# Kernel tuning notes

Measured on AMD Instinct MI355X. Metric: run time of the kernel, lower is better.

## Reference

```python
import jax, jax.numpy as jnp
import numpy as np

B, F_IN, NCH, T = 1, 1, 1536, 128
NW = [476, 476, 292]          # wires per plane (face 0)
NC = [10000, 10000, 10000]    # crossings per plane pair (01, 12, 20)
NCROSS = sum(NC)
E = 120000                    # ~4 nearest-neighbor edges per crossing node
N_FEAT_WIRE = 4
OUT_CH = 4
NODE_DIM = 2 * (F_IN + N_FEAT_WIRE) + 3  # = 13, matches GAT input dim


def setup_inputs() -> dict:
    key = jax.random.key(0)
    ks = jax.random.split(key, 18)
    x = jax.random.normal(ks[0], (B, F_IN, NCH, T), jnp.float32)
    chan_p0 = jax.random.randint(ks[1], (NW[0],), 0, NCH, jnp.int32)
    chan_p1 = jax.random.randint(ks[2], (NW[1],), 0, NCH, jnp.int32)
    chan_p2 = jax.random.randint(ks[3], (NW[2],), 0, NCH, jnp.int32)
    gidx_01 = jax.random.randint(ks[4], (NC[0], 2), 0, min(NW[0], NW[1]), jnp.int32)
    gidx_12 = jax.random.randint(ks[5], (NC[1], 2), 0, min(NW[1], NW[2]), jnp.int32)
    gidx_20 = jax.random.randint(ks[6], (NC[2], 2), 0, min(NW[2], NW[0]), jnp.int32)
    ray_01 = jax.random.normal(ks[7], (NC[0], 2), jnp.float32)
    ray_12 = jax.random.normal(ks[8], (NC[1], 2), jnp.float32)
    ray_20 = jax.random.normal(ks[9], (NC[2], 2), jnp.float32)
    edges = jax.random.randint(ks[10], (2, E), 0, NCROSS, jnp.int32)
    W_gat = jax.random.normal(ks[11], (NODE_DIM, OUT_CH), jnp.float32) * 0.1
    a_src = jax.random.normal(ks[12], (OUT_CH,), jnp.float32) * 0.1
    a_dst = jax.random.normal(ks[13], (OUT_CH,), jnp.float32) * 0.1
    b_gat = jnp.zeros((OUT_CH,), jnp.float32)
    W_mlp = jax.random.normal(ks[14], (OUT_CH, 1), jnp.float32) * 0.1
    b_mlp = jnp.zeros((1,), jnp.float32)
    return dict(x=x, chan_p0=chan_p0, chan_p1=chan_p1, chan_p2=chan_p2,
                gidx_01=gidx_01, gidx_12=gidx_12, gidx_20=gidx_20,
                ray_01=ray_01, ray_12=ray_12, ray_20=ray_20, edges=edges,
                W_gat=W_gat, a_src=a_src, a_dst=a_dst, b_gat=b_gat,
                W_mlp=W_mlp, b_mlp=b_mlp)


def _plane_feats(x, chan, plane_id):
    # x: [B,F,C,T] -> per-wire features [B,T,Nw,F+4]:
    # (signal, wire_ident, channel, 0, plane_id) -- mirrors as_wires_f0_pX.
    sig = jnp.transpose(x[:, :, chan, :], (0, 3, 2, 1))  # [B,T,Nw,F]
    nw = chan.shape[0]
    wire_id = jnp.arange(nw, dtype=jnp.float32)
    extra = jnp.stack([wire_id, chan.astype(jnp.float32),
                       jnp.zeros(nw, jnp.float32),
                       jnp.full((nw,), plane_id, jnp.float32)], axis=-1)  # [Nw,4]
    extra = jnp.broadcast_to(extra[None, None], sig.shape[:2] + extra.shape)
    return jnp.concatenate([sig, extra], axis=-1)


def _cross(fA, fB, gidx, rc):
    # crossing node features: wireA feats ++ wireB feats ++ ray xy ++ tick
    n = gidx.shape[0]
    tick = jnp.broadcast_to(jnp.arange(T, dtype=jnp.float32)[None, :, None, None],
                            (B, T, n, 1))
    rcb = jnp.broadcast_to(rc[None, None], (B, T, n, 2))
    return jnp.concatenate([fA[:, :, gidx[:, 0]], fB[:, :, gidx[:, 1]], rcb, tick],
                           axis=-1)  # [B,T,n,13]


def _gat_one(h, a_src, a_dst, src, dst):
    # single-graph, single-head GAT attention + aggregation. h: [N,OUT_CH]
    s = h @ a_src  # [N]
    d = h @ a_dst
    e = jax.nn.leaky_relu(s[src] + d[dst], 0.2)  # [E]
    m = jax.ops.segment_max(e, dst, num_segments=NCROSS)
    m = jnp.where(jnp.isfinite(m), m, 0.0)
    w = jnp.exp(e - m[dst])
    denom = jax.ops.segment_sum(w, dst, num_segments=NCROSS)
    msg = jax.ops.segment_sum(w[:, None] * h[src], dst, num_segments=NCROSS)
    return msg / (denom[:, None] + 1e-9)


def reference(x, chan_p0, chan_p1, chan_p2, gidx_01, gidx_12, gidx_20,
              ray_01, ray_12, ray_20, edges,
              W_gat, a_src, a_dst, b_gat, W_mlp, b_mlp):
    f0 = _plane_feats(x, chan_p0, 0.0)
    f1 = _plane_feats(x, chan_p1, 1.0)
    f2 = _plane_feats(x, chan_p2, 2.0)
    nodes = jnp.concatenate([_cross(f0, f1, gidx_01, ray_01),
                             _cross(f1, f2, gidx_12, ray_12),
                             _cross(f2, f0, gidx_20, ray_20)], axis=2)  # [B,T,N,13]
    h = nodes @ W_gat + b_gat  # [B,T,N,OUT_CH]
    src, dst = edges[0], edges[1]
    gat = jax.vmap(jax.vmap(lambda hh: _gat_one(hh, a_src, a_dst, src, dst)))
    g = gat(h)  # [B,T,N,OUT_CH]
    return jax.nn.sigmoid(g @ W_mlp + b_mlp)  # [B,T,N,1]
```

## Files before the change

kernel.cpp:

```cpp
#include <hip/hip_runtime.h>

#define T_TICKS 128
#define NCH     1536
#define NCPAIR  10000
#define NCROSS  30000
#define E_EDGES 120000
#define TG      4
#define NTG     (T_TICKS / TG)
#define CAP     32
#define BN      512
#define NBLK    ((NCROSS + BN - 1) / BN)
#define NXPOS   (NTG * NCH)
#define PREP_ITEMS (NCROSS + E_EDGES + NXPOS)


__global__ void k_prep(const float* __restrict__ x,
                       const int* __restrict__ c0, const int* __restrict__ c1,
                       const int* __restrict__ c2,
                       const int* __restrict__ g01, const int* __restrict__ g12,
                       const int* __restrict__ g20,
                       const float* __restrict__ r01,
                       const float* __restrict__ r12,
                       const float* __restrict__ r20,
                       const float* __restrict__ Wg,
                       const float* __restrict__ bg,
                       const float* __restrict__ as_,
                       const float* __restrict__ ad_,
                       const float* __restrict__ Wm,
                       const int* __restrict__ e_src,
                       const int* __restrict__ e_dst,
                       int* __restrict__ counts,
                       int* __restrict__ bucketT,
                       float4* __restrict__ c4,
                       float* __restrict__ dBv,
                       float4* __restrict__ xT4) {
    const int gid = blockIdx.x * 256 + threadIdx.x;
    if (gid < NCROSS) {
        const int n = gid;
        int iA, iB, m;
        float pA, pB;
        const int* cA;
        const int* cB;
        const float* ray;
        if (n < NCPAIR) {
            m = n; cA = c0; cB = c1; pA = 0.f; pB = 1.f; ray = r01;
            iA = g01[2 * m]; iB = g01[2 * m + 1];
        } else if (n < 2 * NCPAIR) {
            m = n - NCPAIR; cA = c1; cB = c2; pA = 1.f; pB = 2.f; ray = r12;
            iA = g12[2 * m]; iB = g12[2 * m + 1];
        } else {
            m = n - 2 * NCPAIR; cA = c2; cB = c0; pA = 2.f; pB = 0.f; ray = r20;
            iA = g20[2 * m]; iB = g20[2 * m + 1];
        }
        const int chA = cA[iA];
        const int chB = cB[iB];
        const float rx = ray[2 * m];
        const float ry = ray[2 * m + 1];

        float base[4];
#pragma unroll
        for (int c = 0; c < 4; c++) {
            base[c] = bg[c]
                    + (float)iA  * Wg[1 * 4 + c] + (float)chA * Wg[2 * 4 + c]
                    + pA         * Wg[4 * 4 + c]
                    + (float)iB  * Wg[6 * 4 + c] + (float)chB * Wg[7 * 4 + c]
                    + pB         * Wg[9 * 4 + c]
                    + rx         * Wg[10 * 4 + c] + ry * Wg[11 * 4 + c];
        }
        float sB = 0.f, dB = 0.f, pBs = 0.f;
#pragma unroll
        for (int c = 0; c < 4; c++) {
            sB  = fmaf(base[c], as_[c], sB);
            dB  = fmaf(base[c], ad_[c], dB);
            pBs = fmaf(base[c], Wm[c], pBs);
        }
        c4[n]  = make_float4(sB, pBs, __int_as_float(chA), __int_as_float(chB));
        dBv[n] = dB;
    } else if (gid < NCROSS + E_EDGES) {
        const int i = gid - NCROSS;
        const int s = e_src[i];
        const int d = e_dst[i];
        const int slot = atomicAdd(&counts[d], 1);
        if (slot < CAP) bucketT[slot * NCROSS + d] = s;
    } else if (gid < PREP_ITEMS) {
        const int i = gid - (NCROSS + E_EDGES);
        const int tg = i / NCH;
        const int c = i - tg * NCH;
        xT4[i] = *(const float4*)(x + c * T_TICKS + tg * TG);
    }
}


__device__ __forceinline__ void upd(float& mx, float& den, float& p,
                                    const float e, const float pj) {
    const float dif = e - mx;
    const float ex = __expf(-fabsf(dif));
    const bool g = dif > 0.f;
    const float scale = g ? ex : 1.f;
    const float w = g ? 1.f : ex;
    mx = g ? e : mx;
    den = fmaf(den, scale, w);
    p = fmaf(p, scale, w * pj);
}

__device__ __forceinline__ void edge_proc(const float4 cs, const float4* xs,
                                          const float sA1, const float sB1,
                                          const float pA1, const float pB1,
                                          const float* ts, const float* tp,
                                          const float* dd,
                                          float* mx, float* den, float* pa) {
    const float4 a4 = xs[__float_as_int(cs.z)];
    const float4 b4 = xs[__float_as_int(cs.w)];
    const float a[4] = {a4.x, a4.y, a4.z, a4.w};
    const float b[4] = {b4.x, b4.y, b4.z, b4.w};
#pragma unroll
    for (int k = 0; k < TG; k++) {
        const float sv = cs.x + a[k] * sA1 + b[k] * sB1 + ts[k];
        const float pv = cs.y + a[k] * pA1 + b[k] * pB1 + tp[k];
        float e = sv + dd[k];
        e = fmaxf(e, 0.2f * e);
        upd(mx[k], den[k], pa[k], e, pv);
    }
}

__global__ __launch_bounds__(512, 8) void k_gat(
        const float4* __restrict__ xT4,
        const float4* __restrict__ c4,
        const float* __restrict__ dBv,
        const int* __restrict__ counts,
        const int* __restrict__ bucketT,
        const float* __restrict__ Wg,
        const float* __restrict__ as_,
        const float* __restrict__ ad_,
        const float* __restrict__ Wm,
        const float* __restrict__ bm,
        float* __restrict__ out) {
    const int lid = blockIdx.x;
    const int xcd = lid & 7;
    const int s   = lid >> 3;
    const int q   = s / NBLK;
    const int nb  = s - q * NBLK;
    const int tg  = xcd + 8 * q;
    const int bbase = nb * BN;
    const int tid = threadIdx.x;
    const int wsz = min(BN, NCROSS - bbase);

    __shared__ float4 xs[NCH];
    __shared__ int perm[BN];
    __shared__ int bins[CAP + 1];
    __shared__ int boff[CAP + 1];
    __shared__ float lres[TG][BN];

    for (int c = tid; c < NCH; c += BN) xs[c] = xT4[tg * NCH + c];

    float sA1 = 0, dA1 = 0, pA1 = 0, sB1 = 0, dB1 = 0, pB1 = 0,
          sT = 0, dT = 0, pT = 0;
#pragma unroll
    for (int c = 0; c < 4; c++) {
        const float va = as_[c], vd = ad_[c], vm = Wm[c];
        const float w0 = Wg[c], w5 = Wg[5 * 4 + c], w12 = Wg[12 * 4 + c];
        sA1 = fmaf(w0, va, sA1);  dA1 = fmaf(w0, vd, dA1);  pA1 = fmaf(w0, vm, pA1);
        sB1 = fmaf(w5, va, sB1);  dB1 = fmaf(w5, vd, dB1);  pB1 = fmaf(w5, vm, pB1);
        sT  = fmaf(w12, va, sT);  dT  = fmaf(w12, vd, dT);  pT  = fmaf(w12, vm, pT);
    }

    int deg0 = 0;
    if (tid < wsz) deg0 = min(counts[bbase + tid], CAP);
    if (tid <= CAP) bins[tid] = 0;
    __syncthreads();
    int lp = 0;
    if (tid < wsz) lp = atomicAdd(&bins[deg0], 1);
    __syncthreads();
    if (tid == 0) {
        int run = 0;
        for (int d = CAP; d >= 0; d--) { boff[d] = run; run += bins[d]; }
    }
    __syncthreads();
    if (tid < wsz) perm[boff[deg0] + lp] = tid;
    __syncthreads();

    if (tid < wsz) {
        const int nloc = perm[tid];
        const int n = bbase + nloc;
        const int deg = min(counts[n], CAP);

        const float4 cc = c4[n];
        const float4 a4 = xs[__float_as_int(cc.z)];
        const float4 b4 = xs[__float_as_int(cc.w)];
        const float dB = dBv[n];
        const float a[4] = {a4.x, a4.y, a4.z, a4.w};
        const float b[4] = {b4.x, b4.y, b4.z, b4.w};

        float dd[TG], ts[TG], tp[TG];
#pragma unroll
        for (int k = 0; k < TG; k++) {
            const float tk = (float)(tg * TG + k);
            dd[k] = dB + a[k] * dA1 + b[k] * dB1 + tk * dT;
            ts[k] = tk * sT;
            tp[k] = tk * pT;
        }
        float mx[TG], den[TG], pa[TG];
#pragma unroll
        for (int k = 0; k < TG; k++) { mx[k] = -INFINITY; den[k] = 0.f; pa[k] = 0.f; }

        const int* bk = bucketT + n;
        int j = 0;
        for (; j + 2 <= deg; j += 2) {
            const int s0 = bk[j * NCROSS];
            const int s1 = bk[(j + 1) * NCROSS];
            const float4 cs0 = c4[s0];
            const float4 cs1 = c4[s1];
            edge_proc(cs0, xs, sA1, sB1, pA1, pB1, ts, tp, dd, mx, den, pa);
            edge_proc(cs1, xs, sA1, sB1, pA1, pB1, ts, tp, dd, mx, den, pa);
        }
        if (j < deg) {
            const int s0 = bk[j * NCROSS];
            const float4 cs0 = c4[s0];
            edge_proc(cs0, xs, sA1, sB1, pA1, pB1, ts, tp, dd, mx, den, pa);
        }

        const float bb = bm[0];
#pragma unroll
        for (int k = 0; k < TG; k++) {
            const float logit = pa[k] / (den[k] + 1e-9f) + bb;
            lres[k][nloc] = 1.f / (1.f + __expf(-logit));
        }
    }
    __syncthreads();
    if (tid < wsz) {
#pragma unroll
        for (int k = 0; k < TG; k++) {
            out[(size_t)(tg * TG + k) * NCROSS + bbase + tid] = lres[k][tid];
        }
    }
}


extern "C" void kernel_launch(void* const* d_in, const int* in_sizes, int n_in,
                              void* d_out, int out_size, void* d_ws, size_t ws_size,
                              hipStream_t stream) {
    const float* x   = (const float*)d_in[0];
    const int* c0  = (const int*)d_in[1];
    const int* c1  = (const int*)d_in[2];
    const int* c2  = (const int*)d_in[3];
    const int* g01 = (const int*)d_in[4];
    const int* g12 = (const int*)d_in[5];
    const int* g20 = (const int*)d_in[6];
    const float* r01 = (const float*)d_in[7];
    const float* r12 = (const float*)d_in[8];
    const float* r20 = (const float*)d_in[9];
    const int* edges = (const int*)d_in[10];
    const float* Wg  = (const float*)d_in[11];
    const float* as_ = (const float*)d_in[12];
    const float* ad_ = (const float*)d_in[13];
    const float* bg  = (const float*)d_in[14];
    const float* Wm  = (const float*)d_in[15];
    const float* bm  = (const float*)d_in[16];
    float* out = (float*)d_out;

    const int* e_src = edges;
    const int* e_dst = edges + E_EDGES;

    char* ws = (char*)d_ws;
    size_t off = 0;
    int* counts = (int*)(ws + off); off += NCROSS * sizeof(int);
    off = (off + 255) & ~(size_t)255;
    int* bucketT = (int*)(ws + off); off += (size_t)CAP * NCROSS * sizeof(int);
    off = (off + 255) & ~(size_t)255;
    float4* c4 = (float4*)(ws + off); off += (size_t)NCROSS * sizeof(float4);
    off = (off + 255) & ~(size_t)255;
    float* dBv = (float*)(ws + off); off += NCROSS * sizeof(float);
    off = (off + 255) & ~(size_t)255;
    float4* xT4 = (float4*)(ws + off); off += (size_t)NXPOS * sizeof(float4);
    (void)ws_size; (void)n_in; (void)in_sizes; (void)out_size;

    hipMemsetAsync(counts, 0, NCROSS * sizeof(int), stream);

    k_prep<<<(PREP_ITEMS + 255) / 256, 256, 0, stream>>>(
        x, c0, c1, c2, g01, g12, g20, r01, r12, r20, Wg, bg, as_, ad_, Wm,
        e_src, e_dst, counts, bucketT, c4, dBv, xT4);

    k_gat<<<NBLK * NTG, BN, 0, stream>>>(xT4, c4, dBv, counts, bucketT,
                                         Wg, as_, ad_, Wm, bm, out);
}
```

Baseline: 136.1 us.

## Store edge buckets node-major, load neighbors as int4, halve block size

Edge buckets move from a slot-major transposed layout to node-major rows of CAP entries. Each thread can then fetch four neighbor indices with a single int4 load and handle up to four edges per iteration with masking. The degree is packed into the perm entry so counts is not re-read. The block size drops from 512 to 256 with a new launch bound. This doubles the block count and changes occupancy, and the masked partial iterations may add divergence.

```diff
diff --git a/kernel.cpp b/kernel.cpp
--- a/kernel.cpp
+++ b/kernel.cpp
@@ -8,7 +8,7 @@
 #define TG      4
 #define NTG     (T_TICKS / TG)
 #define CAP     32
-#define BN      512
+#define BN      256
 #define NBLK    ((NCROSS + BN - 1) / BN)
 #define NXPOS   (NTG * NCH)
 #define PREP_ITEMS (NCROSS + E_EDGES + NXPOS)
@@ -30,7 +30,7 @@
                        const int* __restrict__ e_src,
                        const int* __restrict__ e_dst,
                        int* __restrict__ counts,
-                       int* __restrict__ bucketT,
+                       int* __restrict__ bucket,
                        float4* __restrict__ c4,
                        float* __restrict__ dBv,
                        float4* __restrict__ xT4) {
@@ -81,7 +81,7 @@
         const int s = e_src[i];
         const int d = e_dst[i];
         const int slot = atomicAdd(&counts[d], 1);
-        if (slot < CAP) bucketT[slot * NCROSS + d] = s;
+        if (slot < CAP) bucket[(size_t)d * CAP + slot] = s;
     } else if (gid < PREP_ITEMS) {
         const int i = gid - (NCROSS + E_EDGES);
         const int tg = i / NCH;
@@ -123,12 +123,12 @@
     }
 }
 
-__global__ __launch_bounds__(512, 8) void k_gat(
+__global__ __launch_bounds__(BN, 5) void k_gat(
         const float4* __restrict__ xT4,
         const float4* __restrict__ c4,
         const float* __restrict__ dBv,
         const int* __restrict__ counts,
-        const int* __restrict__ bucketT,
+        const int* __restrict__ bucket,
         const float* __restrict__ Wg,
         const float* __restrict__ as_,
         const float* __restrict__ ad_,
@@ -176,13 +176,14 @@
         for (int d = CAP; d >= 0; d--) { boff[d] = run; run += bins[d]; }
     }
     __syncthreads();
-    if (tid < wsz) perm[boff[deg0] + lp] = tid;
+    if (tid < wsz) perm[boff[deg0] + lp] = tid | (deg0 << 16);
     __syncthreads();
 
     if (tid < wsz) {
-        const int nloc = perm[tid];
+        const int pk = perm[tid];
+        const int nloc = pk & 0xffff;
+        const int deg = pk >> 16;
         const int n = bbase + nloc;
-        const int deg = min(counts[n], CAP);
 
         const float4 cc = c4[n];
         const float4 a4 = xs[__float_as_int(cc.z)];
@@ -203,26 +204,26 @@
 #pragma unroll
         for (int k = 0; k < TG; k++) { mx[k] = -INFINITY; den[k] = 0.f; pa[k] = 0.f; }
 
-        const int* bk = bucketT + n;
-        int j = 0;
-        for (; j + 2 <= deg; j += 2) {
-            const int s0 = bk[j * NCROSS];
-            const int s1 = bk[(j + 1) * NCROSS];
-            const float4 cs0 = c4[s0];
-            const float4 cs1 = c4[s1];
+        const int* bkt = bucket + (size_t)n * CAP;
+        for (int j = 0; j < deg; j += 4) {
+            const int4 bb = *(const int4*)(bkt + j);
+            const int m = deg - j;
+            float4 cs0 = c4[bb.x];
+            float4 cs1 = make_float4(0.f, 0.f, 0.f, 0.f);
+            float4 cs2 = cs1, cs3 = cs1;
+            if (m > 1) cs1 = c4[bb.y];
+            if (m > 2) cs2 = c4[bb.z];
+            if (m > 3) cs3 = c4[bb.w];
             edge_proc(cs0, xs, sA1, sB1, pA1, pB1, ts, tp, dd, mx, den, pa);
-            edge_proc(cs1, xs, sA1, sB1, pA1, pB1, ts, tp, dd, mx, den, pa);
-        }
-        if (j < deg) {
-            const int s0 = bk[j * NCROSS];
-            const float4 cs0 = c4[s0];
-            edge_proc(cs0, xs, sA1, sB1, pA1, pB1, ts, tp, dd, mx, den, pa);
-        }
-
-        const float bb = bm[0];
+            if (m > 1) edge_proc(cs1, xs, sA1, sB1, pA1, pB1, ts, tp, dd, mx, den, pa);
+            if (m > 2) edge_proc(cs2, xs, sA1, sB1, pA1, pB1, ts, tp, dd, mx, den, pa);
+            if (m > 3) edge_proc(cs3, xs, sA1, sB1, pA1, pB1, ts, tp, dd, mx, den, pa);
+        }
+
+        const float bb2 = bm[0];
 #pragma unroll
         for (int k = 0; k < TG; k++) {
-            const float logit = pa[k] / (den[k] + 1e-9f) + bb;
+            const float logit = pa[k] / (den[k] + 1e-9f) + bb2;
             lres[k][nloc] = 1.f / (1.f + __expf(-logit));
         }
     }
@@ -265,7 +266,7 @@
     size_t off = 0;
     int* counts = (int*)(ws + off); off += NCROSS * sizeof(int);
     off = (off + 255) & ~(size_t)255;
-    int* bucketT = (int*)(ws + off); off += (size_t)CAP * NCROSS * sizeof(int);
+    int* bucket = (int*)(ws + off); off += (size_t)NCROSS * CAP * sizeof(int);
     off = (off + 255) & ~(size_t)255;
     float4* c4 = (float4*)(ws + off); off += (size_t)NCROSS * sizeof(float4);
     off = (off + 255) & ~(size_t)255;
@@ -278,8 +279,8 @@
 
     k_prep<<<(PREP_ITEMS + 255) / 256, 256, 0, stream>>>(
         x, c0, c1, c2, g01, g12, g20, r01, r12, r20, Wg, bg, as_, ad_, Wm,
-        e_src, e_dst, counts, bucketT, c4, dBv, xT4);
-
-    k_gat<<<NBLK * NTG, BN, 0, stream>>>(xT4, c4, dBv, counts, bucketT,
+        e_src, e_dst, counts, bucket, c4, dBv, xT4);
+
+    k_gat<<<NBLK * NTG, BN, 0, stream>>>(xT4, c4, dBv, counts, bucket,
                                          Wg, as_, ad_, Wm, bm, out);
 }
```

Result: slower. 146.6 us (+7.7%).
